# Kernel tuning notes

Hardware: AMD Instinct MI355X
Metric: run time of the kernel (lower is better)

## Reference

```python
import jax, jax.numpy as jnp
import numpy as np

B, S, D, H = 32, 2048, 256, 256  # batch, seq_len, input_size, hidden_size


def setup_inputs() -> dict:
    key = jax.random.key(0)
    ks = jax.random.split(key, 9)
    s = 0.05  # small init scale to keep gates in a sane range
    return {
        "inputs": jax.random.normal(ks[0], (B, S, D), dtype=jnp.float32),
        "W_ih0": jax.random.normal(ks[1], (3 * H, D), dtype=jnp.float32) * s,
        "W_hh0": jax.random.normal(ks[2], (3 * H, H), dtype=jnp.float32) * s,
        "b_ih0": jax.random.normal(ks[3], (3 * H,), dtype=jnp.float32) * s,
        "b_hh0": jax.random.normal(ks[4], (3 * H,), dtype=jnp.float32) * s,
        "W_ih1": jax.random.normal(ks[5], (3 * H, 2 * H), dtype=jnp.float32) * s,
        "W_hh1": jax.random.normal(ks[6], (3 * H, H), dtype=jnp.float32) * s,
        "b_ih1": jax.random.normal(ks[7], (3 * H,), dtype=jnp.float32) * s,
        "b_hh1": jax.random.normal(ks[8], (3 * H,), dtype=jnp.float32) * s,
    }


def _gru_scan(gx, W_hh, b_hh, reverse):
    """gx: [S,B,3H] precomputed input projections. Returns ([S,B,H] states in
    original time order, [B,H] final carry). lax.scan(reverse=True) stores
    outputs at matching time positions, which matches the module's flip(1)."""
    Hh = W_hh.shape[1]
    h0 = jnp.zeros((gx.shape[1], Hh), gx.dtype)

    def step(h, gx_t):
        gh = h @ W_hh.T + b_hh                      # [B,3H]
        xr, xz, xn = jnp.split(gx_t, 3, axis=-1)
        hr, hz, hn = jnp.split(gh, 3, axis=-1)
        r = jax.nn.sigmoid(xr + hr)
        z = jax.nn.sigmoid(xz + hz)
        n = jnp.tanh(xn + r * hn)
        h_new = (1.0 - z) * n + z * h               # torch.nn.GRUCell update
        return h_new, h_new

    h_last, hs = jax.lax.scan(step, h0, gx, reverse=reverse)
    return hs, h_last


def _bidir_layer(x, W_ih, W_hh, b_ih, b_hh):
    # Precompute all input-to-hidden GEMMs in one batched matmul.
    gx = jnp.einsum('bsd,gd->sbg', x, W_ih) + b_ih  # [S,B,3H]
    # cells_backward is a deepcopy of cells_forward -> identical weights.
    hs_f, hf = _gru_scan(gx, W_hh, b_hh, reverse=False)
    hs_b, hb = _gru_scan(gx, W_hh, b_hh, reverse=True)
    out = jnp.concatenate([hs_f, hs_b], axis=-1).transpose(1, 0, 2)  # [B,S,2H]
    return out, hf, hb


def reference(inputs, W_ih0, W_hh0, b_ih0, b_hh0, W_ih1, W_hh1, b_ih1, b_hh1):
    out0, hf0, hb0 = _bidir_layer(inputs, W_ih0, W_hh0, b_ih0, b_hh0)
    out1, hf1, hb1 = _bidir_layer(out0, W_ih1, W_hh1, b_ih1, b_hh1)
    # h_n order: (layer0 fwd, layer0 bwd, layer1 fwd, layer1 bwd)
    h_n = jnp.stack([hf0, hb0, hf1, hb1])           # [layers*dirs, B, H]
    return out1, h_n
```

## Files before the change

kernel.cpp:

```cpp
#include <hip/hip_runtime.h>

typedef __attribute__((ext_vector_type(4))) float f32x4;
typedef __attribute__((ext_vector_type(8))) short bf16x8;
typedef __attribute__((ext_vector_type(4))) _Float16 f16x4;

constexpr int kB = 32;
constexpr int kS = 2048;
constexpr int kH = 256;
constexpr int kG = 768;

__device__ __forceinline__ short f2bf(float f) {
  unsigned u = __builtin_bit_cast(unsigned, f);
  u += 0x7fffu + ((u >> 16) & 1u);
  return (short)(u >> 16);
}

__device__ __forceinline__ float fast_sigmoid(float x) {
  float e = __builtin_amdgcn_exp2f(x * 1.4426950408889634f);
  return e * __builtin_amdgcn_rcpf(1.0f + e);
}
__device__ __forceinline__ float fast_tanh(float x) {
  float e = __builtin_amdgcn_exp2f(x * 2.8853900817779268f);
  return 1.0f - 2.0f * __builtin_amdgcn_rcpf(1.0f + e);
}

__device__ __forceinline__ void load8(const float* p, float v[8]) {
  const float4 a = *(const float4*)p;
  const float4 b = *(const float4*)(p + 4);
  v[0] = a.x; v[1] = a.y; v[2] = a.z; v[3] = a.w;
  v[4] = b.x; v[5] = b.y; v[6] = b.z; v[7] = b.w;
}

template <int LAYER>
__global__ __launch_bounds__(256) void gemm_gx(
    const void* __restrict__ Av, const float* __restrict__ W,
    const float* __restrict__ b_ih, const float* __restrict__ b_hh,
    _Float16* __restrict__ gx) {
  constexpr int K = (LAYER == 0) ? 256 : 512;
  __shared__ short As[64][40];
  __shared__ short Ws[64][40];
  const int tid = threadIdx.x;
  const int lane = tid & 63, wv = tid >> 6;
  const int quad = lane >> 4, l15 = lane & 15;
  const int m0 = blockIdx.y * 64, n0 = blockIdx.x * 64;
  const int srow = tid >> 2, kq = tid & 3;
  const int am = m0 + srow;
  const int b = am & 31, s = am >> 5;
  const float* Wrow = W + (size_t)(n0 + srow) * K;
  const float* Af = (const float*)Av + ((size_t)b * kS + s) * 256;
  const short* Ab = (const short*)Av + ((size_t)s * 64 + b) * 256;

  f32x4 acc[4] = {};

  for (int k0 = 0; k0 < K; k0 += 32) {
    const int k = k0 + kq * 8;
    short avs[8];
    if constexpr (LAYER == 0) {
      float v[8];
      load8(Af + k, v);
#pragma unroll
      for (int j = 0; j < 8; ++j) avs[j] = f2bf(v[j]);
    } else {
      *(uint4*)avs = *(const uint4*)(Ab + (size_t)(k >> 8) * 8192 + (k & 255));
    }
    float wv8[8];
    load8(Wrow + k, wv8);
    __syncthreads();
#pragma unroll
    for (int j = 0; j < 8; ++j) As[srow][kq * 8 + j] = avs[j];
#pragma unroll
    for (int j = 0; j < 8; ++j) Ws[srow][kq * 8 + j] = f2bf(wv8[j]);
    __syncthreads();
    const bf16x8 bf = *(const bf16x8*)&Ws[wv * 16 + l15][quad * 8];
#pragma unroll
    for (int mt = 0; mt < 4; ++mt) {
      const bf16x8 af = *(const bf16x8*)&As[mt * 16 + l15][quad * 8];
      acc[mt] = __builtin_amdgcn_mfma_f32_16x16x32_bf16(af, bf, acc[mt], 0, 0, 0);
    }
  }
  const int col = n0 + wv * 16 + l15;
  const float bias = b_ih[col] + (col < 512 ? b_hh[col] : 0.0f);
#pragma unroll
  for (int mt = 0; mt < 4; ++mt) {
#pragma unroll
    for (int r = 0; r < 4; ++r) {
      const int m = m0 + mt * 16 + quad * 4 + r;
      gx[((size_t)(m >> 5) * kG + col) * 32 + (m & 31)] = (_Float16)(acc[mt][r] + bias);
    }
  }
}

union Frag8 {
  bf16x8 v;
  uint2 u2[2];
};

template <int LAYER>
__global__ __launch_bounds__(512, 2) void gru_scan(
    const _Float16* __restrict__ gx,
    const float* __restrict__ W_hh,
    const float* __restrict__ b_hh,
    void* __restrict__ outv,
    float* __restrict__ hn) {
  __shared__ short hlds[16][264];
  __shared__ short wlds[768][36];

  const int tid = threadIdx.x;
  const int lane = tid & 63;
  const int w = tid >> 6;
  const int quad = lane >> 4, l15 = lane & 15;
  const int dir = blockIdx.x & 1;
  const int bbase = (blockIdx.x >> 1) * 16;

  for (int i = tid; i < 16 * 264; i += 512) (&hlds[0][0])[i] = 0;

  {
    const int kq = tid & 3, rb = tid >> 2;
#pragma unroll
    for (int j = 0; j < 6; ++j) {
      const int row = rb + j * 128;
      float v[8];
      load8(W_hh + (size_t)row * kH + 224 + kq * 8, v);
#pragma unroll
      for (int e = 0; e < 8; ++e) wlds[row][kq * 8 + e] = f2bf(v[e]);
    }
  }

  const int colH0 = w * 32 + l15;
  bf16x8 Bf[3][2][7];
#pragma unroll
  for (int g3 = 0; g3 < 3; ++g3)
#pragma unroll
    for (int nt = 0; nt < 2; ++nt)
#pragma unroll
      for (int kb = 0; kb < 7; ++kb) {
        const int row = g3 * 256 + colH0 + nt * 16;
        float v[8];
        load8(W_hh + (size_t)row * kH + kb * 32 + quad * 8, v);
        bf16x8 f;
#pragma unroll
        for (int e = 0; e < 8; ++e) f[e] = f2bf(v[e]);
        Bf[g3][nt][kb] = f;
      }

  const float bhn[2] = {b_hh[512 + colH0], b_hh[512 + colH0 + 16]};
  float hprev[8] = {0, 0, 0, 0, 0, 0, 0, 0};

  short* out0 = (short*)outv;
  float* out1 = (float*)outv;

  __syncthreads();

  for (int i = 0; i < kS; ++i) {
    const int t = dir ? (kS - 1 - i) : i;
    const _Float16* gxt = gx + (size_t)t * (kG * 32);

    f16x4 gxv[3][2];
#pragma unroll
    for (int g3 = 0; g3 < 3; ++g3)
#pragma unroll
      for (int nt = 0; nt < 2; ++nt)
        gxv[g3][nt] = *(const f16x4*)(gxt + (size_t)(g3 * 256 + colH0 + nt * 16) * 32 +
                                      bbase + quad * 4);

    f32x4 C0[2] = {}, C1[2] = {}, C2[2] = {};

#define CHAIN(G3, CC)                                                              \
  {                                                                                \
    _Pragma("unroll") for (int kb = 0; kb < 7; ++kb) {                             \
      const bf16x8 af = *(const bf16x8*)&hlds[l15][kb * 32 + quad * 8];            \
      _Pragma("unroll") for (int nt = 0; nt < 2; ++nt) CC[nt] =                    \
          __builtin_amdgcn_mfma_f32_16x16x32_bf16(af, Bf[G3][nt][kb], CC[nt], 0, 0, 0); \
    }                                                                              \
    const bf16x8 af7 = *(const bf16x8*)&hlds[l15][224 + quad * 8];                 \
    _Pragma("unroll") for (int nt = 0; nt < 2; ++nt) {                             \
      Frag8 bf;                                                                    \
      const int row = G3 * 256 + colH0 + nt * 16;                                  \
      bf.u2[0] = *(const uint2*)&wlds[row][quad * 8];                              \
      bf.u2[1] = *(const uint2*)&wlds[row][quad * 8 + 4];                          \
      CC[nt] = __builtin_amdgcn_mfma_f32_16x16x32_bf16(af7, bf.v, CC[nt], 0, 0, 0); \
    }                                                                              \
  }

    CHAIN(0, C0)
    CHAIN(2, C2)

    float rr[2][4];
#pragma unroll
    for (int nt = 0; nt < 2; ++nt)
#pragma unroll
      for (int r = 0; r < 4; ++r)
        rr[nt][r] = fast_sigmoid((float)gxv[0][nt][r] + C0[nt][r]);

    CHAIN(1, C1)

    float nn[2][4];
#pragma unroll
    for (int nt = 0; nt < 2; ++nt)
#pragma unroll
      for (int r = 0; r < 4; ++r)
        nn[nt][r] = fast_tanh((float)gxv[2][nt][r] + rr[nt][r] * (C2[nt][r] + bhn[nt]));

    __syncthreads();

#pragma unroll
    for (int nt = 0; nt < 2; ++nt) {
#pragma unroll
      for (int r = 0; r < 4; ++r) {
        const float zz = fast_sigmoid((float)gxv[1][nt][r] + C1[nt][r]);
        const int e = nt * 4 + r;
        const float h = nn[nt][r] + zz * (hprev[e] - nn[nt][r]);
        hprev[e] = h;
        hlds[quad * 4 + r][colH0 + nt * 16] = f2bf(h);
        if constexpr (LAYER == 1) {
          out1[((size_t)(bbase + quad * 4 + r) * kS + t) * 512 + dir * 256 + colH0 +
               nt * 16] = h;
        }
      }
    }
    __syncthreads();

    if constexpr (LAYER == 0) {
      const int srow = tid >> 5, schunk = tid & 31;
      *(uint4*)(out0 + (((size_t)t * 2 + dir) * 32 + bbase + srow) * 256 + schunk * 8) =
          *(const uint4*)&hlds[srow][schunk * 8];
    }
  }
#undef CHAIN

#pragma unroll
  for (int nt = 0; nt < 2; ++nt)
#pragma unroll
    for (int r = 0; r < 4; ++r)
      hn[(size_t)(dir * kB + bbase + quad * 4 + r) * kH + colH0 + nt * 16] =
          hprev[nt * 4 + r];
}

extern "C" void kernel_launch(void* const* d_in, const int* in_sizes, int n_in,
                              void* d_out, int out_size, void* d_ws, size_t ws_size,
                              hipStream_t stream) {
  const float* x     = (const float*)d_in[0];
  const float* W_ih0 = (const float*)d_in[1];
  const float* W_hh0 = (const float*)d_in[2];
  const float* b_ih0 = (const float*)d_in[3];
  const float* b_hh0 = (const float*)d_in[4];
  const float* W_ih1 = (const float*)d_in[5];
  const float* W_hh1 = (const float*)d_in[6];
  const float* b_ih1 = (const float*)d_in[7];
  const float* b_hh1 = (const float*)d_in[8];

  float* out1 = (float*)d_out;
  float* hn = out1 + (size_t)kB * kS * 512;

  _Float16* gxb = (_Float16*)d_ws;
  short* out0 = (short*)((char*)d_ws + (size_t)kS * kB * kG * 2);

  dim3 ggrid(kG / 64, (kS * kB) / 64);

  gemm_gx<0><<<ggrid, 256, 0, stream>>>(x, W_ih0, b_ih0, b_hh0, gxb);
  gru_scan<0><<<dim3(4), 512, 0, stream>>>(gxb, W_hh0, b_hh0, out0, hn);
  gemm_gx<1><<<ggrid, 256, 0, stream>>>(out0, W_ih1, b_ih1, b_hh1, gxb);
  gru_scan<1><<<dim3(4), 512, 0, stream>>>(gxb, W_hh1, b_hh1, out1, hn + 2 * kB * kH);
}
```

Measured before the change: 7.833 ms.

## Double-buffer hidden state, prefetch next gx, keep all W_hh fragments in registers

Double-buffers the hidden-state LDS tile so each timestep needs one barrier instead of two. The next step's gx values are prefetched one iteration ahead. The last K-block of W_hh moves from LDS into registers (8 fragments per gate), and the r and n gate MFMAs are interleaved. It also uses packed bf16 conversion and a cheaper sigmoid. The cost is higher register pressure from the larger weight fragment array at 512 threads with 2 blocks per CU, which could cause spills.

```diff
diff --git a/kernel.cpp b/kernel.cpp
--- a/kernel.cpp
+++ b/kernel.cpp
@@ -15,9 +15,14 @@
   return (short)(u >> 16);
 }
 
+__device__ __forceinline__ unsigned cvt_pk_bf16(float lo, float hi) {
+  unsigned r;
+  asm("v_cvt_pk_bf16_f32 %0, %1, %2" : "=v"(r) : "v"(lo), "v"(hi));
+  return r;
+}
+
 __device__ __forceinline__ float fast_sigmoid(float x) {
-  float e = __builtin_amdgcn_exp2f(x * 1.4426950408889634f);
-  return e * __builtin_amdgcn_rcpf(1.0f + e);
+  return __builtin_amdgcn_rcpf(1.0f + __builtin_amdgcn_exp2f(x * -1.4426950408889634f));
 }
 __device__ __forceinline__ float fast_tanh(float x) {
   float e = __builtin_amdgcn_exp2f(x * 2.8853900817779268f);
@@ -90,11 +95,6 @@
   }
 }
 
-union Frag8 {
-  bf16x8 v;
-  uint2 u2[2];
-};
-
 template <int LAYER>
 __global__ __launch_bounds__(512, 2) void gru_scan(
     const _Float16* __restrict__ gx,
@@ -102,8 +102,7 @@
     const float* __restrict__ b_hh,
     void* __restrict__ outv,
     float* __restrict__ hn) {
-  __shared__ short hlds[16][264];
-  __shared__ short wlds[768][36];
+  __shared__ short hlds[2][16][264];
 
   const int tid = threadIdx.x;
   const int lane = tid & 63;
@@ -112,28 +111,17 @@
   const int dir = blockIdx.x & 1;
   const int bbase = (blockIdx.x >> 1) * 16;
 
-  for (int i = tid; i < 16 * 264; i += 512) (&hlds[0][0])[i] = 0;
-
-  {
-    const int kq = tid & 3, rb = tid >> 2;
-#pragma unroll
-    for (int j = 0; j < 6; ++j) {
-      const int row = rb + j * 128;
-      float v[8];
-      load8(W_hh + (size_t)row * kH + 224 + kq * 8, v);
-#pragma unroll
-      for (int e = 0; e < 8; ++e) wlds[row][kq * 8 + e] = f2bf(v[e]);
-    }
-  }
+  for (int i = tid; i < 2 * 16 * 264; i += 512) (&hlds[0][0][0])[i] = 0;
 
   const int colH0 = w * 32 + l15;
-  bf16x8 Bf[3][2][7];
+
+  bf16x8 Bf[3][2][8];
 #pragma unroll
   for (int g3 = 0; g3 < 3; ++g3)
 #pragma unroll
     for (int nt = 0; nt < 2; ++nt)
 #pragma unroll
-      for (int kb = 0; kb < 7; ++kb) {
+      for (int kb = 0; kb < 8; ++kb) {
         const int row = g3 * 256 + colH0 + nt * 16;
         float v[8];
         load8(W_hh + (size_t)row * kH + kb * 32 + quad * 8, v);
@@ -149,84 +137,119 @@
   short* out0 = (short*)outv;
   float* out1 = (float*)outv;
 
+  size_t gxoff[3][2];
+#pragma unroll
+  for (int g3 = 0; g3 < 3; ++g3)
+#pragma unroll
+    for (int nt = 0; nt < 2; ++nt)
+      gxoff[g3][nt] =
+          (size_t)(g3 * 256 + colH0 + nt * 16) * 32 + bbase + quad * 4;
+
+  f16x4 gxv[3][2];
+  {
+    const int t0 = dir ? (kS - 1) : 0;
+    const _Float16* gxt = gx + (size_t)t0 * (kG * 32);
+#pragma unroll
+    for (int g3 = 0; g3 < 3; ++g3)
+#pragma unroll
+      for (int nt = 0; nt < 2; ++nt)
+        gxv[g3][nt] = *(const f16x4*)(gxt + gxoff[g3][nt]);
+  }
+
   __syncthreads();
 
   for (int i = 0; i < kS; ++i) {
     const int t = dir ? (kS - 1 - i) : i;
-    const _Float16* gxt = gx + (size_t)t * (kG * 32);
-
-    f16x4 gxv[3][2];
-#pragma unroll
-    for (int g3 = 0; g3 < 3; ++g3)
+    const short(*hbuf)[264] = hlds[i & 1];
+    short(*hnext)[264] = hlds[(i & 1) ^ 1];
+
+    f16x4 gxn[3][2];
+    {
+      const int i2 = (i + 1 < kS) ? (i + 1) : i;
+      const int t2 = dir ? (kS - 1 - i2) : i2;
+      const _Float16* gxt2 = gx + (size_t)t2 * (kG * 32);
+#pragma unroll
+      for (int g3 = 0; g3 < 3; ++g3)
+#pragma unroll
+        for (int nt = 0; nt < 2; ++nt)
+          gxn[g3][nt] = *(const f16x4*)(gxt2 + gxoff[g3][nt]);
+    }
+
+    f32x4 accR[2] = {}, accZ[2] = {}, accN[2] = {};
+
+#pragma unroll
+    for (int kb = 0; kb < 8; ++kb) {
+      const bf16x8 af = *(const bf16x8*)&hbuf[l15][kb * 32 + quad * 8];
+#pragma unroll
+      for (int nt = 0; nt < 2; ++nt) {
+        accR[nt] =
+            __builtin_amdgcn_mfma_f32_16x16x32_bf16(af, Bf[0][nt][kb], accR[nt], 0, 0, 0);
+        accN[nt] =
+            __builtin_amdgcn_mfma_f32_16x16x32_bf16(af, Bf[2][nt][kb], accN[nt], 0, 0, 0);
+      }
+    }
+
+    float rr[2][4];
+#pragma unroll
+    for (int nt = 0; nt < 2; ++nt)
+#pragma unroll
+      for (int r = 0; r < 4; ++r)
+        rr[nt][r] = fast_sigmoid((float)gxv[0][nt][r] + accR[nt][r]);
+
+#pragma unroll
+    for (int kb = 0; kb < 8; ++kb) {
+      const bf16x8 af = *(const bf16x8*)&hbuf[l15][kb * 32 + quad * 8];
 #pragma unroll
       for (int nt = 0; nt < 2; ++nt)
-        gxv[g3][nt] = *(const f16x4*)(gxt + (size_t)(g3 * 256 + colH0 + nt * 16) * 32 +
-                                      bbase + quad * 4);
-
-    f32x4 C0[2] = {}, C1[2] = {}, C2[2] = {};
-
-#define CHAIN(G3, CC)                                                              \
-  {                                                                                \
-    _Pragma("unroll") for (int kb = 0; kb < 7; ++kb) {                             \
-      const bf16x8 af = *(const bf16x8*)&hlds[l15][kb * 32 + quad * 8];            \
-      _Pragma("unroll") for (int nt = 0; nt < 2; ++nt) CC[nt] =                    \
-          __builtin_amdgcn_mfma_f32_16x16x32_bf16(af, Bf[G3][nt][kb], CC[nt], 0, 0, 0); \
-    }                                                                              \
-    const bf16x8 af7 = *(const bf16x8*)&hlds[l15][224 + quad * 8];                 \
-    _Pragma("unroll") for (int nt = 0; nt < 2; ++nt) {                             \
-      Frag8 bf;                                                                    \
-      const int row = G3 * 256 + colH0 + nt * 16;                                  \
-      bf.u2[0] = *(const uint2*)&wlds[row][quad * 8];                              \
-      bf.u2[1] = *(const uint2*)&wlds[row][quad * 8 + 4];                          \
-      CC[nt] = __builtin_amdgcn_mfma_f32_16x16x32_bf16(af7, bf.v, CC[nt], 0, 0, 0); \
-    }                                                                              \
-  }
-
-    CHAIN(0, C0)
-    CHAIN(2, C2)
-
-    float rr[2][4];
+        accZ[nt] =
+            __builtin_amdgcn_mfma_f32_16x16x32_bf16(af, Bf[1][nt][kb], accZ[nt], 0, 0, 0);
+    }
+
+    float nn[2][4];
 #pragma unroll
     for (int nt = 0; nt < 2; ++nt)
 #pragma unroll
       for (int r = 0; r < 4; ++r)
-        rr[nt][r] = fast_sigmoid((float)gxv[0][nt][r] + C0[nt][r]);
-
-    CHAIN(1, C1)
-
-    float nn[2][4];
-#pragma unroll
-    for (int nt = 0; nt < 2; ++nt)
-#pragma unroll
-      for (int r = 0; r < 4; ++r)
-        nn[nt][r] = fast_tanh((float)gxv[2][nt][r] + rr[nt][r] * (C2[nt][r] + bhn[nt]));
-
-    __syncthreads();
+        nn[nt][r] =
+            fast_tanh((float)gxv[2][nt][r] + rr[nt][r] * (accN[nt][r] + bhn[nt]));
 
 #pragma unroll
     for (int nt = 0; nt < 2; ++nt) {
+      float hv[4];
 #pragma unroll
       for (int r = 0; r < 4; ++r) {
-        const float zz = fast_sigmoid((float)gxv[1][nt][r] + C1[nt][r]);
+        const float zz = fast_sigmoid((float)gxv[1][nt][r] + accZ[nt][r]);
         const int e = nt * 4 + r;
         const float h = nn[nt][r] + zz * (hprev[e] - nn[nt][r]);
         hprev[e] = h;
-        hlds[quad * 4 + r][colH0 + nt * 16] = f2bf(h);
+        hv[r] = h;
         if constexpr (LAYER == 1) {
           out1[((size_t)(bbase + quad * 4 + r) * kS + t) * 512 + dir * 256 + colH0 +
                nt * 16] = h;
         }
       }
-    }
+      const unsigned u01 = cvt_pk_bf16(hv[0], hv[1]);
+      const unsigned u23 = cvt_pk_bf16(hv[2], hv[3]);
+      const int col = colH0 + nt * 16;
+      hnext[quad * 4 + 0][col] = (short)u01;
+      hnext[quad * 4 + 1][col] = (short)(u01 >> 16);
+      hnext[quad * 4 + 2][col] = (short)u23;
+      hnext[quad * 4 + 3][col] = (short)(u23 >> 16);
+    }
+
+#pragma unroll
+    for (int g3 = 0; g3 < 3; ++g3)
+#pragma unroll
+      for (int nt = 0; nt < 2; ++nt) gxv[g3][nt] = gxn[g3][nt];
+
     __syncthreads();
 
     if constexpr (LAYER == 0) {
       const int srow = tid >> 5, schunk = tid & 31;
       *(uint4*)(out0 + (((size_t)t * 2 + dir) * 32 + bbase + srow) * 256 + schunk * 8) =
-          *(const uint4*)&hlds[srow][schunk * 8];
-    }
-  }
-#undef CHAIN
+          *(const uint4*)&hlds[(i & 1) ^ 1][srow][schunk * 8];
+    }
+  }
 
 #pragma unroll
   for (int nt = 0; nt < 2; ++nt)
```

After: 10.67 ms. +36.2%, slower.
